# Performance work log

Hardware: AMD Instinct MI355X
Metric: run time of the kernel (lower is better)

Reference implementation:

```python
import jax, jax.numpy as jnp
import numpy as np

BETA = 0.25

def setup_inputs() -> dict:
    key = jax.random.key(0)
    k1, k2 = jax.random.split(key)
    B, D, H, W = 32, 64, 64, 64
    K = 512
    z_e = jax.random.normal(k1, (B, D, H, W), dtype=jnp.float32)
    emb = jax.random.uniform(k2, (K, D), dtype=jnp.float32, minval=-1.0 / K, maxval=1.0 / K)
    return {"z_e": z_e, "emb": emb}

def reference(z_e, emb):
    B, D, H, W = z_e.shape
    K = emb.shape[0]
    # flatten to [N, D] tokens (channels-last)
    z = jnp.transpose(z_e, (0, 2, 3, 1)).reshape(-1, D)
    # squared euclidean distances [N, K] via expansion
    dist = (jnp.sum(z * z, axis=1, keepdims=True)
            + jnp.sum(emb * emb, axis=1)[None, :]
            - 2.0 * (z @ emb.T))
    indices = jnp.argmin(dist, axis=1)  # [N]
    z_q = emb[indices].reshape(B, H, W, D)
    z_q = jnp.transpose(z_q, (0, 3, 1, 2))  # [B, D, H, W]
    # losses: mse * D (torch F.mse_loss averages over all elements)
    loss_codebook = jnp.mean((z_q - jax.lax.stop_gradient(z_e)) ** 2) * D
    loss_commit = jnp.mean((z_e - jax.lax.stop_gradient(z_q)) ** 2) * D
    loss_vq = loss_codebook + BETA * loss_commit
    # straight-through estimator
    z_q_st = z_e + jax.lax.stop_gradient(z_q - z_e)
    # usage stats
    counts = jnp.bincount(indices, length=K)
    total = jnp.maximum(1, jnp.sum(counts))
    probs = counts.astype(jnp.float32) / total.astype(jnp.float32)
    ent = -jnp.sum(jnp.where(probs > 0, probs * jnp.log(jnp.where(probs > 0, probs, 1.0)), 0.0))
    perplexity = jnp.exp(ent)
    codes_used = jnp.sum(counts > 0)
    usage_ratio = codes_used.astype(jnp.float32) / K
    avg_dist2 = jnp.mean(jnp.min(dist, axis=1))
    return (z_q_st, loss_vq, perplexity, codes_used, usage_ratio, avg_dist2,
            indices.reshape(B, H, W))
```

## Files before the change

kernel.cpp:

```cpp
#include <hip/hip_runtime.h>


#define NTOK 131072
#define DDIM 64
#define KCB  512
#define KQ   128
#define HWSZ 4096

__global__ void vq_see_kernel(const float* __restrict__ emb,
                              float* __restrict__ see) {
  int k = blockIdx.x * 64 + threadIdx.x;
  if (k < KCB) {
    const float* e = emb + k * DDIM;
    float s = 0.f;
#pragma unroll
    for (int d = 0; d < DDIM; ++d) s = fmaf(e[d], e[d], s);
    see[k] = s;
  }
}

__global__ __launch_bounds__(256, 2) void vq_search_kernel(
    const float* __restrict__ z_e, const float* __restrict__ emb,
    const float* __restrict__ see, float2* __restrict__ pairs) {
  __shared__ float4 ldsE[KQ][16];
  __shared__ float  ldsS[KQ];

  const int tid = threadIdx.x;
  const int kq  = blockIdx.x & 3;
  const int tb  = blockIdx.x >> 2;
  const int kqbase = kq * KQ;

  {
    const float4* src = reinterpret_cast<const float4*>(emb) + kqbase * 16;
    float4* dst = &ldsE[0][0];
#pragma unroll
    for (int v = tid; v < KQ * 16; v += 256) dst[v] = src[v];
    if (tid < KQ) ldsS[tid] = see[kqbase + tid];
  }
  __syncthreads();

  float z[2][DDIM];
  float szz[2];
#pragma unroll
  for (int t = 0; t < 2; ++t) {
    const int tok = tb * 512 + t * 256 + tid;
    const int b   = tok >> 12;
    const int hw  = tok & 4095;
    const float* zp = z_e + (size_t)b * DDIM * HWSZ + hw;
#pragma unroll
    for (int d = 0; d < DDIM; ++d) z[t][d] = zp[(size_t)d * HWSZ];
    float s = 0.f;
#pragma unroll
    for (int d = 0; d < DDIM; ++d) s = fmaf(z[t][d], z[t][d], s);
    szz[t] = s;
  }

  float best[2] = {3.4e38f, 3.4e38f};
  int   bidx[2] = {kqbase, kqbase};

  for (int kk = 0; kk < KQ; kk += 2) {
    float a00 = 0.f, a01 = 0.f, a10 = 0.f, a11 = 0.f;
    const float4* e0p = ldsE[kk + 0];
    const float4* e1p = ldsE[kk + 1];
#pragma unroll
    for (int dv = 0; dv < 16; ++dv) {
      const float4 e0 = e0p[dv];
      const float4 e1 = e1p[dv];
      const float z00 = z[0][4 * dv + 0], z01 = z[0][4 * dv + 1];
      const float z02 = z[0][4 * dv + 2], z03 = z[0][4 * dv + 3];
      const float z10 = z[1][4 * dv + 0], z11 = z[1][4 * dv + 1];
      const float z12 = z[1][4 * dv + 2], z13 = z[1][4 * dv + 3];
      a00 = fmaf(z00, e0.x, a00); a00 = fmaf(z01, e0.y, a00);
      a00 = fmaf(z02, e0.z, a00); a00 = fmaf(z03, e0.w, a00);
      a01 = fmaf(z00, e1.x, a01); a01 = fmaf(z01, e1.y, a01);
      a01 = fmaf(z02, e1.z, a01); a01 = fmaf(z03, e1.w, a01);
      a10 = fmaf(z10, e0.x, a10); a10 = fmaf(z11, e0.y, a10);
      a10 = fmaf(z12, e0.z, a10); a10 = fmaf(z13, e0.w, a10);
      a11 = fmaf(z10, e1.x, a11); a11 = fmaf(z11, e1.y, a11);
      a11 = fmaf(z12, e1.z, a11); a11 = fmaf(z13, e1.w, a11);
    }
    const float se0 = ldsS[kk + 0];
    const float se1 = ldsS[kk + 1];
    const int   kg  = kqbase + kk;
    float d;
    d = (szz[0] + se0) - 2.f * a00; if (d < best[0]) { best[0] = d; bidx[0] = kg; }
    d = (szz[0] + se1) - 2.f * a01; if (d < best[0]) { best[0] = d; bidx[0] = kg + 1; }
    d = (szz[1] + se0) - 2.f * a10; if (d < best[1]) { best[1] = d; bidx[1] = kg; }
    d = (szz[1] + se1) - 2.f * a11; if (d < best[1]) { best[1] = d; bidx[1] = kg + 1; }
  }

#pragma unroll
  for (int t = 0; t < 2; ++t) {
    const int tok = tb * 512 + t * 256 + tid;
    float2 p;
    p.x = best[t];
    p.y = __int_as_float(bidx[t]);
    pairs[(size_t)kq * NTOK + tok] = p;
  }
}

__global__ __launch_bounds__(256) void vq_epilogue_kernel(
    const float* __restrict__ z_e, const float* __restrict__ emb,
    const float2* __restrict__ pairs, float* __restrict__ out,
    float* __restrict__ out_idx, int* __restrict__ counts,
    double* __restrict__ sums) {
  __shared__ int hist[KCB];
  __shared__ double sq_s[4];
  __shared__ double md_s[4];

  const int tid = threadIdx.x;
#pragma unroll
  for (int i = tid; i < KCB; i += 256) hist[i] = 0;
  __syncthreads();

  const int tok = blockIdx.x * 256 + tid;
  const int b   = tok >> 12;
  const int hw  = tok & 4095;

  float best = 3.4e38f;
  int   bidx = 0;
#pragma unroll
  for (int q = 0; q < 4; ++q) {
    const float2 p = pairs[(size_t)q * NTOK + tok];
    if (p.x < best) { best = p.x; bidx = __float_as_int(p.y); }
  }

  atomicAdd(&hist[bidx], 1);

  const float* zp = z_e + (size_t)b * DDIM * HWSZ + hw;
  float* op = out + (size_t)b * DDIM * HWSZ + hw;
  const float4* eq = reinterpret_cast<const float4*>(emb + bidx * DDIM);

  double sq = 0.0;
#pragma unroll
  for (int d4 = 0; d4 < 16; ++d4) {
    const float4 q = eq[d4];
    const float zq[4] = {q.x, q.y, q.z, q.w};
#pragma unroll
    for (int c = 0; c < 4; ++c) {
      const int d = 4 * d4 + c;
      const float ze  = zp[(size_t)d * HWSZ];
      const float df  = zq[c] - ze;
      const float val = ze + df;
      op[(size_t)d * HWSZ] = val;
      sq = fma((double)df, (double)df, sq);
    }
  }

  out_idx[tok] = (float)bidx;

  double md = (double)best;
#pragma unroll
  for (int off = 32; off > 0; off >>= 1) {
    sq += __shfl_down(sq, off);
    md += __shfl_down(md, off);
  }
  const int wave = tid >> 6;
  if ((tid & 63) == 0) { sq_s[wave] = sq; md_s[wave] = md; }
  __syncthreads();
  if (tid == 0) {
    double tsq = sq_s[0] + sq_s[1] + sq_s[2] + sq_s[3];
    double tmd = md_s[0] + md_s[1] + md_s[2] + md_s[3];
    unsafeAtomicAdd(&sums[0], tsq);
    unsafeAtomicAdd(&sums[1], tmd);
  }

  for (int i = tid; i < KCB; i += 256) {
    const int h = hist[i];
    if (h) atomicAdd(&counts[i], h);
  }
}

__global__ void vq_final_kernel(const int* __restrict__ counts,
                                const double* __restrict__ sums,
                                float* __restrict__ scal) {
  __shared__ double ent_s[8];
  __shared__ int    used_s[8];
  const int tid = threadIdx.x;
  const int c = counts[tid];
  const double p = (double)c / 131072.0;
  double e = (c > 0) ? (-p * log(p)) : 0.0;
  int u = (c > 0) ? 1 : 0;
#pragma unroll
  for (int off = 32; off > 0; off >>= 1) {
    e += __shfl_down(e, off);
    u += __shfl_down(u, off);
  }
  if ((tid & 63) == 0) { ent_s[tid >> 6] = e; used_s[tid >> 6] = u; }
  __syncthreads();
  if (tid == 0) {
    double ent = 0.0; int used = 0;
#pragma unroll
    for (int w = 0; w < 8; ++w) { ent += ent_s[w]; used += used_s[w]; }
    const double mse = sums[0] / 8388608.0;
    scal[0] = (float)(mse * 64.0 * 1.25);
    scal[1] = (float)exp(ent);
    scal[2] = (float)used;
    scal[3] = (float)used / 512.f;
    scal[4] = (float)(sums[1] / 131072.0);
  }
}

extern "C" void kernel_launch(void* const* d_in, const int* in_sizes, int n_in,
                              void* d_out, int out_size, void* d_ws,
                              size_t ws_size, hipStream_t stream) {
  const float* z_e = (const float*)d_in[0];
  const float* emb = (const float*)d_in[1];
  float* out = (float*)d_out;

  double* sums   = (double*)d_ws;
  int*    counts = (int*)((char*)d_ws + 16);
  float*  see    = (float*)((char*)d_ws + 2064);
  float2* pairs  = (float2*)((char*)d_ws + 4608);

  hipMemsetAsync(d_ws, 0, 2064, stream);
  vq_see_kernel<<<8, 64, 0, stream>>>(emb, see);
  vq_search_kernel<<<1024, 256, 0, stream>>>(z_e, emb, see, pairs);
  vq_epilogue_kernel<<<512, 256, 0, stream>>>(z_e, emb, pairs, out,
                                              out + 8388613, counts, sums);
  vq_final_kernel<<<1, 512, 0, stream>>>(counts, sums, out + 8388608);
}
```

Before: 231.6 us.

## Raise search occupancy with one token per thread and split epilogue over channels

```diff
diff --git a/kernel.cpp b/kernel.cpp
--- a/kernel.cpp
+++ b/kernel.cpp
@@ -5,6 +5,7 @@
 #define DDIM 64
 #define KCB  512
 #define KQ   128
+#define NSPLIT 4
 #define HWSZ 4096
 
 __global__ void vq_see_kernel(const float* __restrict__ emb,
@@ -19,15 +20,16 @@
   }
 }
 
-__global__ __launch_bounds__(256, 2) void vq_search_kernel(
+__global__ __launch_bounds__(256, 4) void vq_search_kernel(
     const float* __restrict__ z_e, const float* __restrict__ emb,
     const float* __restrict__ see, float2* __restrict__ pairs) {
   __shared__ float4 ldsE[KQ][16];
   __shared__ float  ldsS[KQ];
 
   const int tid = threadIdx.x;
-  const int kq  = blockIdx.x & 3;
-  const int tb  = blockIdx.x >> 2;
+  const int x   = blockIdx.x;
+  const int tb  = (x & 7) | ((x >> 5) << 3);
+  const int kq  = (x >> 3) & 3;
   const int kqbase = kq * KQ;
 
   {
@@ -39,64 +41,60 @@
   }
   __syncthreads();
 
-  float z[2][DDIM];
-  float szz[2];
-#pragma unroll
-  for (int t = 0; t < 2; ++t) {
-    const int tok = tb * 512 + t * 256 + tid;
-    const int b   = tok >> 12;
-    const int hw  = tok & 4095;
-    const float* zp = z_e + (size_t)b * DDIM * HWSZ + hw;
-#pragma unroll
-    for (int d = 0; d < DDIM; ++d) z[t][d] = zp[(size_t)d * HWSZ];
-    float s = 0.f;
-#pragma unroll
-    for (int d = 0; d < DDIM; ++d) s = fmaf(z[t][d], z[t][d], s);
-    szz[t] = s;
-  }
-
-  float best[2] = {3.4e38f, 3.4e38f};
-  int   bidx[2] = {kqbase, kqbase};
-
-  for (int kk = 0; kk < KQ; kk += 2) {
-    float a00 = 0.f, a01 = 0.f, a10 = 0.f, a11 = 0.f;
+  const int tok = tb * 256 + tid;
+  const int b   = tok >> 12;
+  const int hw  = tok & 4095;
+  const float* zp = z_e + (size_t)b * DDIM * HWSZ + hw;
+
+  float z[DDIM];
+#pragma unroll
+  for (int d = 0; d < DDIM; ++d) z[d] = zp[(size_t)d * HWSZ];
+
+  float szz = 0.f;
+#pragma unroll
+  for (int d = 0; d < DDIM; ++d) szz = fmaf(z[d], z[d], szz);
+
+#pragma unroll
+  for (int d = 0; d < DDIM; ++d) asm volatile("" : "+v"(z[d]));
+
+  float best = 3.4e38f;
+  int   bidx = kqbase;
+
+  for (int kk = 0; kk < KQ; kk += 4) {
+    float a0 = 0.f, a1 = 0.f, a2 = 0.f, a3 = 0.f;
     const float4* e0p = ldsE[kk + 0];
     const float4* e1p = ldsE[kk + 1];
+    const float4* e2p = ldsE[kk + 2];
+    const float4* e3p = ldsE[kk + 3];
 #pragma unroll
     for (int dv = 0; dv < 16; ++dv) {
       const float4 e0 = e0p[dv];
       const float4 e1 = e1p[dv];
-      const float z00 = z[0][4 * dv + 0], z01 = z[0][4 * dv + 1];
-      const float z02 = z[0][4 * dv + 2], z03 = z[0][4 * dv + 3];
-      const float z10 = z[1][4 * dv + 0], z11 = z[1][4 * dv + 1];
-      const float z12 = z[1][4 * dv + 2], z13 = z[1][4 * dv + 3];
-      a00 = fmaf(z00, e0.x, a00); a00 = fmaf(z01, e0.y, a00);
-      a00 = fmaf(z02, e0.z, a00); a00 = fmaf(z03, e0.w, a00);
-      a01 = fmaf(z00, e1.x, a01); a01 = fmaf(z01, e1.y, a01);
-      a01 = fmaf(z02, e1.z, a01); a01 = fmaf(z03, e1.w, a01);
-      a10 = fmaf(z10, e0.x, a10); a10 = fmaf(z11, e0.y, a10);
-      a10 = fmaf(z12, e0.z, a10); a10 = fmaf(z13, e0.w, a10);
-      a11 = fmaf(z10, e1.x, a11); a11 = fmaf(z11, e1.y, a11);
-      a11 = fmaf(z12, e1.z, a11); a11 = fmaf(z13, e1.w, a11);
+      const float4 e2 = e2p[dv];
+      const float4 e3 = e3p[dv];
+      const float z0 = z[4 * dv + 0], z1 = z[4 * dv + 1];
+      const float z2 = z[4 * dv + 2], z3 = z[4 * dv + 3];
+      a0 = fmaf(z0, e0.x, a0); a0 = fmaf(z1, e0.y, a0);
+      a0 = fmaf(z2, e0.z, a0); a0 = fmaf(z3, e0.w, a0);
+      a1 = fmaf(z0, e1.x, a1); a1 = fmaf(z1, e1.y, a1);
+      a1 = fmaf(z2, e1.z, a1); a1 = fmaf(z3, e1.w, a1);
+      a2 = fmaf(z0, e2.x, a2); a2 = fmaf(z1, e2.y, a2);
+      a2 = fmaf(z2, e2.z, a2); a2 = fmaf(z3, e2.w, a2);
+      a3 = fmaf(z0, e3.x, a3); a3 = fmaf(z1, e3.y, a3);
+      a3 = fmaf(z2, e3.z, a3); a3 = fmaf(z3, e3.w, a3);
     }
-    const float se0 = ldsS[kk + 0];
-    const float se1 = ldsS[kk + 1];
-    const int   kg  = kqbase + kk;
+    const int kg = kqbase + kk;
     float d;
-    d = (szz[0] + se0) - 2.f * a00; if (d < best[0]) { best[0] = d; bidx[0] = kg; }
-    d = (szz[0] + se1) - 2.f * a01; if (d < best[0]) { best[0] = d; bidx[0] = kg + 1; }
-    d = (szz[1] + se0) - 2.f * a10; if (d < best[1]) { best[1] = d; bidx[1] = kg; }
-    d = (szz[1] + se1) - 2.f * a11; if (d < best[1]) { best[1] = d; bidx[1] = kg + 1; }
-  }
-
-#pragma unroll
-  for (int t = 0; t < 2; ++t) {
-    const int tok = tb * 512 + t * 256 + tid;
-    float2 p;
-    p.x = best[t];
-    p.y = __int_as_float(bidx[t]);
-    pairs[(size_t)kq * NTOK + tok] = p;
-  }
+    d = (szz + ldsS[kk + 0]) - 2.f * a0; if (d < best) { best = d; bidx = kg; }
+    d = (szz + ldsS[kk + 1]) - 2.f * a1; if (d < best) { best = d; bidx = kg + 1; }
+    d = (szz + ldsS[kk + 2]) - 2.f * a2; if (d < best) { best = d; bidx = kg + 2; }
+    d = (szz + ldsS[kk + 3]) - 2.f * a3; if (d < best) { best = d; bidx = kg + 3; }
+  }
+
+  float2 p;
+  p.x = best;
+  p.y = __int_as_float(bidx);
+  pairs[(size_t)kq * NTOK + tok] = p;
 }
 
 __global__ __launch_bounds__(256) void vq_epilogue_kernel(
@@ -104,36 +102,36 @@
     const float2* __restrict__ pairs, float* __restrict__ out,
     float* __restrict__ out_idx, int* __restrict__ counts,
     double* __restrict__ sums) {
-  __shared__ int hist[KCB];
   __shared__ double sq_s[4];
   __shared__ double md_s[4];
 
   const int tid = threadIdx.x;
-#pragma unroll
-  for (int i = tid; i < KCB; i += 256) hist[i] = 0;
-  __syncthreads();
-
-  const int tok = blockIdx.x * 256 + tid;
+  const int dq  = tid >> 6;
+  const int tok = blockIdx.x * 64 + (tid & 63);
   const int b   = tok >> 12;
   const int hw  = tok & 4095;
 
   float best = 3.4e38f;
   int   bidx = 0;
 #pragma unroll
-  for (int q = 0; q < 4; ++q) {
+  for (int q = 0; q < NSPLIT; ++q) {
     const float2 p = pairs[(size_t)q * NTOK + tok];
     if (p.x < best) { best = p.x; bidx = __float_as_int(p.y); }
   }
 
-  atomicAdd(&hist[bidx], 1);
-
-  const float* zp = z_e + (size_t)b * DDIM * HWSZ + hw;
-  float* op = out + (size_t)b * DDIM * HWSZ + hw;
-  const float4* eq = reinterpret_cast<const float4*>(emb + bidx * DDIM);
+  if (dq == 0) {
+    atomicAdd(&counts[bidx], 1);
+    out_idx[tok] = (float)bidx;
+  }
+
+  const size_t base = (size_t)b * DDIM * HWSZ + hw + (size_t)(dq * 16) * HWSZ;
+  const float* zp = z_e + base;
+  float* op = out + base;
+  const float4* eq = reinterpret_cast<const float4*>(emb + bidx * DDIM) + dq * 4;
 
   double sq = 0.0;
 #pragma unroll
-  for (int d4 = 0; d4 < 16; ++d4) {
+  for (int d4 = 0; d4 < 4; ++d4) {
     const float4 q = eq[d4];
     const float zq[4] = {q.x, q.y, q.z, q.w};
 #pragma unroll
@@ -147,9 +145,7 @@
     }
   }
 
-  out_idx[tok] = (float)bidx;
-
-  double md = (double)best;
+  double md = (dq == 0) ? (double)best : 0.0;
 #pragma unroll
   for (int off = 32; off > 0; off >>= 1) {
     sq += __shfl_down(sq, off);
@@ -163,11 +159,6 @@
     double tmd = md_s[0] + md_s[1] + md_s[2] + md_s[3];
     unsafeAtomicAdd(&sums[0], tsq);
     unsafeAtomicAdd(&sums[1], tmd);
-  }
-
-  for (int i = tid; i < KCB; i += 256) {
-    const int h = hist[i];
-    if (h) atomicAdd(&counts[i], h);
   }
 }
 
@@ -215,8 +206,8 @@
 
   hipMemsetAsync(d_ws, 0, 2064, stream);
   vq_see_kernel<<<8, 64, 0, stream>>>(emb, see);
-  vq_search_kernel<<<1024, 256, 0, stream>>>(z_e, emb, see, pairs);
-  vq_epilogue_kernel<<<512, 256, 0, stream>>>(z_e, emb, pairs, out,
-                                              out + 8388613, counts, sums);
+  vq_search_kernel<<<2048, 256, 0, stream>>>(z_e, emb, see, pairs);
+  vq_epilogue_kernel<<<2048, 256, 0, stream>>>(z_e, emb, pairs, out,
+                                               out + 8388613, counts, sums);
   vq_final_kernel<<<1, 512, 0, stream>>>(counts, sums, out + 8388608);
 }
```

Measured after the change: 299.4 us. +29.3%, slower.

## Fuse codebook search and epilogue into one kernel with split-D token mapping

Applied to the files above, without the earlier changes.

```diff
diff --git a/kernel.cpp b/kernel.cpp
--- a/kernel.cpp
+++ b/kernel.cpp
@@ -4,8 +4,10 @@
 #define NTOK 131072
 #define DDIM 64
 #define KCB  512
-#define KQ   128
 #define HWSZ 4096
+#define CHUNK 128
+#define NCHUNK 4
+#define THREADS 1024
 
 __global__ void vq_see_kernel(const float* __restrict__ emb,
                               float* __restrict__ see) {
@@ -19,153 +21,123 @@
   }
 }
 
-__global__ __launch_bounds__(256, 2) void vq_search_kernel(
+__global__ __launch_bounds__(THREADS, 4) void vq_fused_kernel(
     const float* __restrict__ z_e, const float* __restrict__ emb,
-    const float* __restrict__ see, float2* __restrict__ pairs) {
-  __shared__ float4 ldsE[KQ][16];
-  __shared__ float  ldsS[KQ];
-
-  const int tid = threadIdx.x;
-  const int kq  = blockIdx.x & 3;
-  const int tb  = blockIdx.x >> 2;
-  const int kqbase = kq * KQ;
-
-  {
-    const float4* src = reinterpret_cast<const float4*>(emb) + kqbase * 16;
-    float4* dst = &ldsE[0][0];
-#pragma unroll
-    for (int v = tid; v < KQ * 16; v += 256) dst[v] = src[v];
-    if (tid < KQ) ldsS[tid] = see[kqbase + tid];
-  }
-  __syncthreads();
-
-  float z[2][DDIM];
-  float szz[2];
-#pragma unroll
-  for (int t = 0; t < 2; ++t) {
-    const int tok = tb * 512 + t * 256 + tid;
-    const int b   = tok >> 12;
-    const int hw  = tok & 4095;
-    const float* zp = z_e + (size_t)b * DDIM * HWSZ + hw;
-#pragma unroll
-    for (int d = 0; d < DDIM; ++d) z[t][d] = zp[(size_t)d * HWSZ];
-    float s = 0.f;
-#pragma unroll
-    for (int d = 0; d < DDIM; ++d) s = fmaf(z[t][d], z[t][d], s);
-    szz[t] = s;
-  }
-
-  float best[2] = {3.4e38f, 3.4e38f};
-  int   bidx[2] = {kqbase, kqbase};
-
-  for (int kk = 0; kk < KQ; kk += 2) {
-    float a00 = 0.f, a01 = 0.f, a10 = 0.f, a11 = 0.f;
-    const float4* e0p = ldsE[kk + 0];
-    const float4* e1p = ldsE[kk + 1];
-#pragma unroll
-    for (int dv = 0; dv < 16; ++dv) {
-      const float4 e0 = e0p[dv];
-      const float4 e1 = e1p[dv];
-      const float z00 = z[0][4 * dv + 0], z01 = z[0][4 * dv + 1];
-      const float z02 = z[0][4 * dv + 2], z03 = z[0][4 * dv + 3];
-      const float z10 = z[1][4 * dv + 0], z11 = z[1][4 * dv + 1];
-      const float z12 = z[1][4 * dv + 2], z13 = z[1][4 * dv + 3];
-      a00 = fmaf(z00, e0.x, a00); a00 = fmaf(z01, e0.y, a00);
-      a00 = fmaf(z02, e0.z, a00); a00 = fmaf(z03, e0.w, a00);
-      a01 = fmaf(z00, e1.x, a01); a01 = fmaf(z01, e1.y, a01);
-      a01 = fmaf(z02, e1.z, a01); a01 = fmaf(z03, e1.w, a01);
-      a10 = fmaf(z10, e0.x, a10); a10 = fmaf(z11, e0.y, a10);
-      a10 = fmaf(z12, e0.z, a10); a10 = fmaf(z13, e0.w, a10);
-      a11 = fmaf(z10, e1.x, a11); a11 = fmaf(z11, e1.y, a11);
-      a11 = fmaf(z12, e1.z, a11); a11 = fmaf(z13, e1.w, a11);
-    }
-    const float se0 = ldsS[kk + 0];
-    const float se1 = ldsS[kk + 1];
-    const int   kg  = kqbase + kk;
-    float d;
-    d = (szz[0] + se0) - 2.f * a00; if (d < best[0]) { best[0] = d; bidx[0] = kg; }
-    d = (szz[0] + se1) - 2.f * a01; if (d < best[0]) { best[0] = d; bidx[0] = kg + 1; }
-    d = (szz[1] + se0) - 2.f * a10; if (d < best[1]) { best[1] = d; bidx[1] = kg; }
-    d = (szz[1] + se1) - 2.f * a11; if (d < best[1]) { best[1] = d; bidx[1] = kg + 1; }
-  }
-
-#pragma unroll
-  for (int t = 0; t < 2; ++t) {
-    const int tok = tb * 512 + t * 256 + tid;
-    float2 p;
-    p.x = best[t];
-    p.y = __int_as_float(bidx[t]);
-    pairs[(size_t)kq * NTOK + tok] = p;
-  }
-}
-
-__global__ __launch_bounds__(256) void vq_epilogue_kernel(
-    const float* __restrict__ z_e, const float* __restrict__ emb,
-    const float2* __restrict__ pairs, float* __restrict__ out,
+    const float* __restrict__ see, float* __restrict__ out,
     float* __restrict__ out_idx, int* __restrict__ counts,
     double* __restrict__ sums) {
-  __shared__ int hist[KCB];
-  __shared__ double sq_s[4];
-  __shared__ double md_s[4];
+  __shared__ float  ldsE[CHUNK * DDIM];
+  __shared__ float  ldsS[KCB];
+  __shared__ int    hist[KCB];
+  __shared__ double sq_s[16];
+  __shared__ double md_s[16];
 
-  const int tid = threadIdx.x;
+  const int tid   = threadIdx.x;
+  const int tok16 = tid & 15;
+  const int dch   = (tid >> 4) & 3;
+  const int wv    = tid >> 6;
+  const int tok   = blockIdx.x * 256 + wv * 16 + tok16;
+  const int b     = tok >> 12;
+  const int hw    = tok & 4095;
+  const int d0    = dch * 16;
+
+  for (int i = tid; i < KCB; i += THREADS) { hist[i] = 0; ldsS[i] = see[i]; }
+
+  const float* zp = z_e + (size_t)b * (DDIM * HWSZ) + (size_t)d0 * HWSZ + hw;
+  float z[16];
 #pragma unroll
-  for (int i = tid; i < KCB; i += 256) hist[i] = 0;
-  __syncthreads();
+  for (int j = 0; j < 16; ++j) z[j] = zp[(size_t)j * HWSZ];
 
-  const int tok = blockIdx.x * 256 + tid;
-  const int b   = tok >> 12;
-  const int hw  = tok & 4095;
+  float pz = 0.f;
+#pragma unroll
+  for (int j = 0; j < 16; ++j) pz = fmaf(z[j], z[j], pz);
+  float t1 = pz + __shfl_xor(pz, 16, 64);
+  const float szz = t1 + __shfl_xor(t1, 32, 64);
 
   float best = 3.4e38f;
   int   bidx = 0;
+
+  for (int ch = 0; ch < NCHUNK; ++ch) {
+    __syncthreads();
+    {
+      const float4* src =
+          reinterpret_cast<const float4*>(emb + ch * (CHUNK * DDIM));
+      float4* dst = reinterpret_cast<float4*>(ldsE);
 #pragma unroll
-  for (int q = 0; q < 4; ++q) {
-    const float2 p = pairs[(size_t)q * NTOK + tok];
-    if (p.x < best) { best = p.x; bidx = __float_as_int(p.y); }
+      for (int v = tid; v < CHUNK * DDIM / 4; v += THREADS) dst[v] = src[v];
+    }
+    __syncthreads();
+
+    const int kb = ch * CHUNK;
+#pragma unroll 1
+    for (int kk = 0; kk < CHUNK; kk += 8) {
+      float a[8];
+#pragma unroll
+      for (int c = 0; c < 8; ++c) {
+        const float4* ep =
+            reinterpret_cast<const float4*>(ldsE + (kk + c) * DDIM + d0);
+        float acc = 0.f;
+#pragma unroll
+        for (int j4 = 0; j4 < 4; ++j4) {
+          const float4 e = ep[j4];
+          acc = fmaf(z[4 * j4 + 0], e.x, acc);
+          acc = fmaf(z[4 * j4 + 1], e.y, acc);
+          acc = fmaf(z[4 * j4 + 2], e.z, acc);
+          acc = fmaf(z[4 * j4 + 3], e.w, acc);
+        }
+        a[c] = acc;
+      }
+#pragma unroll
+      for (int c = 0; c < 8; ++c) {
+        const float s1  = a[c] + __shfl_xor(a[c], 16, 64);
+        const float dot = s1 + __shfl_xor(s1, 32, 64);
+        const int   k   = kb + kk + c;
+        const float dist = (szz + ldsS[k]) - 2.f * dot;
+        if (dist < best) { best = dist; bidx = k; }
+      }
+    }
   }
 
-  atomicAdd(&hist[bidx], 1);
+  if (dch == 0) {
+    atomicAdd(&hist[bidx], 1);
+    out_idx[tok] = (float)bidx;
+  }
 
-  const float* zp = z_e + (size_t)b * DDIM * HWSZ + hw;
-  float* op = out + (size_t)b * DDIM * HWSZ + hw;
-  const float4* eq = reinterpret_cast<const float4*>(emb + bidx * DDIM);
+  const float4* eq =
+      reinterpret_cast<const float4*>(emb + bidx * DDIM + d0);
+  float* op = out + (size_t)b * (DDIM * HWSZ) + (size_t)d0 * HWSZ + hw;
 
   double sq = 0.0;
 #pragma unroll
-  for (int d4 = 0; d4 < 16; ++d4) {
-    const float4 q = eq[d4];
-    const float zq[4] = {q.x, q.y, q.z, q.w};
+  for (int j4 = 0; j4 < 4; ++j4) {
+    const float4 e = eq[j4];
+    const float zq[4] = {e.x, e.y, e.z, e.w};
 #pragma unroll
-    for (int c = 0; c < 4; ++c) {
-      const int d = 4 * d4 + c;
-      const float ze  = zp[(size_t)d * HWSZ];
-      const float df  = zq[c] - ze;
-      const float val = ze + df;
-      op[(size_t)d * HWSZ] = val;
+    for (int c2 = 0; c2 < 4; ++c2) {
+      const int j = j4 * 4 + c2;
+      const float df  = zq[c2] - z[j];
+      const float val = z[j] + df;
+      op[(size_t)j * HWSZ] = val;
       sq = fma((double)df, (double)df, sq);
     }
   }
 
-  out_idx[tok] = (float)bidx;
-
-  double md = (double)best;
+  double md = (dch == 0) ? (double)best : 0.0;
 #pragma unroll
   for (int off = 32; off > 0; off >>= 1) {
     sq += __shfl_down(sq, off);
     md += __shfl_down(md, off);
   }
-  const int wave = tid >> 6;
-  if ((tid & 63) == 0) { sq_s[wave] = sq; md_s[wave] = md; }
+  if ((tid & 63) == 0) { sq_s[wv] = sq; md_s[wv] = md; }
   __syncthreads();
   if (tid == 0) {
-    double tsq = sq_s[0] + sq_s[1] + sq_s[2] + sq_s[3];
-    double tmd = md_s[0] + md_s[1] + md_s[2] + md_s[3];
+    double tsq = 0.0, tmd = 0.0;
+#pragma unroll
+    for (int w = 0; w < 16; ++w) { tsq += sq_s[w]; tmd += md_s[w]; }
     unsafeAtomicAdd(&sums[0], tsq);
     unsafeAtomicAdd(&sums[1], tmd);
   }
-
-  for (int i = tid; i < KCB; i += 256) {
+  for (int i = tid; i < KCB; i += THREADS) {
     const int h = hist[i];
     if (h) atomicAdd(&counts[i], h);
   }
@@ -211,12 +183,10 @@
   double* sums   = (double*)d_ws;
   int*    counts = (int*)((char*)d_ws + 16);
   float*  see    = (float*)((char*)d_ws + 2064);
-  float2* pairs  = (float2*)((char*)d_ws + 4608);
 
   hipMemsetAsync(d_ws, 0, 2064, stream);
   vq_see_kernel<<<8, 64, 0, stream>>>(emb, see);
-  vq_search_kernel<<<1024, 256, 0, stream>>>(z_e, emb, see, pairs);
-  vq_epilogue_kernel<<<512, 256, 0, stream>>>(z_e, emb, pairs, out,
-                                              out + 8388613, counts, sums);
+  vq_fused_kernel<<<NTOK / 256, THREADS, 0, stream>>>(
+      z_e, emb, see, out, out + 8388613, counts, sums);
   vq_final_kernel<<<1, 512, 0, stream>>>(counts, sums, out + 8388608);
 }
```

Result: slower. 328.0 us (+41.6%).
